# Performance work log

Measured on AMD Instinct MI355X. Metric: run time of the kernel, lower is better.

The kernel has to match this reference:

```python
import jax, jax.numpy as jnp
import numpy as np

LN_EPS = 1e-5


def setup_inputs() -> dict:
    key = jax.random.key(0)
    ks = jax.random.split(key, 5)
    B, L, D, H = 4, 4096, 2048, 16
    s = 0.02  # keep activations in a sane range for fp32
    return {
        "x": jax.random.normal(ks[0], (B, L, D), jnp.float32),
        "Wq": jax.random.normal(ks[1], (D, D), jnp.float32) * s,
        "Wv": jax.random.normal(ks[2], (D, D), jnp.float32) * s,
        "Wg": jax.random.normal(ks[3], (D, D), jnp.float32) * s,
        "Wo": jax.random.normal(ks[4], (D, D), jnp.float32) * s,
        "beta": jnp.full((H,), -0.2, jnp.float32),  # module init: _beta = -0.2
        "ln_w": jnp.ones((D,), jnp.float32),
        "ln_b": jnp.zeros((D,), jnp.float32),
    }


def _retention_scan(v, lam):
    # v: (B, L, H, Dh); lam: (H,). state_t = lam * state_{t-1} + v_t
    B, L, H, Dh = v.shape
    a = jnp.broadcast_to(lam[None, None, :, None], (B, L, H, 1))

    def combine(c1, c2):
        a1, b1 = c1
        a2, b2 = c2
        return (a1 * a2, b1 * a2 + b2)

    _, state = jax.lax.associative_scan(combine, (a, v), axis=1)
    return state  # (B, L, H, Dh)


def reference(x, Wq, Wv, Wg, Wo, beta, ln_w, ln_b):
    B, L, D = x.shape
    H = beta.shape[0]
    Dh = D // H
    # bias-free projections (torch Linear: x @ W.T)
    q = (x @ Wq.T).reshape(B, L, H, Dh)
    v = (x @ Wv.T).reshape(B, L, H, Dh)
    lam = jax.nn.sigmoid(beta)  # per-head decay, (H,)
    state = _retention_scan(v, lam)  # decay-weighted cumulative sum
    y = (q * state).reshape(B, L, D)
    # LayerNorm over d_model
    mu = jnp.mean(y, axis=-1, keepdims=True)
    var = jnp.mean(jnp.square(y - mu), axis=-1, keepdims=True)
    y = (y - mu) * jax.lax.rsqrt(var + LN_EPS) * ln_w + ln_b
    # SiLU gate
    y = y * jax.nn.silu(x @ Wg.T)
    return y @ Wo.T
```

## Files before the change

### kernel.cpp

```cpp
#include <hip/hip_runtime.h>

#define BATCH 4
#define SEQ   4096
#define DMODEL 2048
#define NHEAD 16
#define DHEAD 128
#define MROWS (BATCH*SEQ)
#define LC    128
#define NCH   (SEQ/LC)

typedef unsigned short ushort_t;
typedef __bf16 v8bf __attribute__((ext_vector_type(8)));
typedef float  f32x4 __attribute__((ext_vector_type(4)));

__device__ __forceinline__ float b2f(ushort_t h) {
    return __uint_as_float(((unsigned)h) << 16);
}
__device__ __forceinline__ ushort_t f2b(float f) {
    unsigned u = __float_as_uint(f);
    return (ushort_t)((u + 0x7fffu + ((u >> 16) & 1u)) >> 16);
}

__global__ void cast_f32_bf16(const float* __restrict__ in, ushort_t* __restrict__ out, int n) {
    int i = (blockIdx.x * blockDim.x + threadIdx.x) * 8;
    const int stride = gridDim.x * blockDim.x * 8;
    for (; i < n; i += stride) {
        float4 a = *(const float4*)(in + i);
        float4 b = *(const float4*)(in + i + 4);
        ushort_t o[8] = {f2b(a.x), f2b(a.y), f2b(a.z), f2b(a.w),
                         f2b(b.x), f2b(b.y), f2b(b.z), f2b(b.w)};
        *(uint4*)(out + i) = *(const uint4*)o;
    }
}

__global__ void cast_weights(const float* __restrict__ w0, const float* __restrict__ w1,
                             const float* __restrict__ w2, const float* __restrict__ w3,
                             ushort_t* __restrict__ o0, ushort_t* __restrict__ o1,
                             ushort_t* __restrict__ o2, ushort_t* __restrict__ o3) {
    const int wsel = blockIdx.y;
    const float* src = wsel == 0 ? w0 : wsel == 1 ? w1 : wsel == 2 ? w2 : w3;
    ushort_t* dst    = wsel == 0 ? o0 : wsel == 1 ? o1 : wsel == 2 ? o2 : o3;
    const int n = DMODEL * DMODEL;
    int i = (blockIdx.x * blockDim.x + threadIdx.x) * 8;
    const int stride = gridDim.x * blockDim.x * 8;
    for (; i < n; i += stride) {
        float4 a = *(const float4*)(src + i);
        float4 b = *(const float4*)(src + i + 4);
        ushort_t o[8] = {f2b(a.x), f2b(a.y), f2b(a.z), f2b(a.w),
                         f2b(b.x), f2b(b.y), f2b(b.z), f2b(b.w)};
        *(uint4*)(dst + i) = *(const uint4*)o;
    }
}


#define GLL(src, dstoff) __builtin_amdgcn_global_load_lds( \
    (const __attribute__((address_space(1))) void*)(src), \
    (__attribute__((address_space(3))) void*)((char*)lds + (dstoff)), 16, 0, 0)

#define STG_A(buf, half, kt) do { \
    GLL(pA + ((half) * 128 +  0) * (size_t)K + (kt), (buf) * 65536 + (half) * 16384 + wid * 1024); \
    GLL(pA + ((half) * 128 + 64) * (size_t)K + (kt), (buf) * 65536 + (half) * 16384 + wid * 1024 + 8192); } while (0)
#define STG_B(buf, half, kt) do { \
    GLL(pB + ((half) * 128 +  0) * (size_t)K + (kt), (buf) * 65536 + 32768 + (half) * 16384 + wid * 1024); \
    GLL(pB + ((half) * 128 + 64) * (size_t)K + (kt), (buf) * 65536 + 32768 + (half) * 16384 + wid * 1024 + 8192); } while (0)

#define DSRD4(dst, off) do { \
    const ushort_t* _p = lds + (off); \
    dst[0] = *(const v8bf*)_p;          dst[1] = *(const v8bf*)(_p + 1024); \
    dst[2] = *(const v8bf*)(_p + 2048); dst[3] = *(const v8bf*)(_p + 3072); } while (0)

#define VMW(n) asm volatile("s_waitcnt vmcnt(" #n ")" ::: "memory")
#define BAR()  __builtin_amdgcn_s_barrier()

#define MM(mh, va, vb) do { \
    __builtin_amdgcn_s_setprio(1); \
    _Pragma("unroll") \
    for (int _m = 0; _m < 4; ++_m) \
        _Pragma("unroll") \
        for (int _n = 0; _n < 4; ++_n) \
            acc[(mh) * 4 + _m][_n] = __builtin_amdgcn_mfma_f32_16x16x32_bf16( \
                va[_m], vb[_n], acc[(mh) * 4 + _m][_n], 0, 0, 0); \
    __builtin_amdgcn_s_setprio(0); \
} while (0)

template<int N, int EPI>
__global__ __launch_bounds__(512, 2) void gemm8(const ushort_t* __restrict__ A,
                                                const ushort_t* __restrict__ Bm,
                                                ushort_t* __restrict__ o0,
                                                ushort_t* __restrict__ o1,
                                                ushort_t* __restrict__ o2,
                                                float* __restrict__ of) {
    constexpr int K  = DMODEL;
    constexpr int NT = K / 64;
    constexpr int NBN = N / 256;
    constexpr int NWG = (MROWS / 256) * NBN;
    extern __shared__ ushort_t lds[];

    int wg = blockIdx.x;
    wg = (wg & 7) * (NWG / 8) + (wg >> 3);
    const int tm = (wg / NBN) * 256;
    const int tn = (wg % NBN) * 256;

    const int tid  = threadIdx.x;
    const int lane = tid & 63;
    const int wid  = tid >> 6;
    const int wr   = wid >> 2;
    const int wc   = wid & 3;

    const int rs = wid * 8 + (lane >> 3);
    const int cs = ((lane & 7) ^ ((lane >> 3) & 7)) * 8;
    const ushort_t* pA = A  + (size_t)(tm + rs) * K + cs;
    const ushort_t* pB = Bm + (size_t)(tn + rs) * K + cs;

    const int q  = lane >> 4;
    const int l4 = lane & 15;
    const int sx = l4 & 7;
    const int abase0 = (wr * 128 + l4) * 64 + ((q ^ sx)) * 8;
    const int abase1 = (wr * 128 + l4) * 64 + (((4 + q) ^ sx)) * 8;
    const int bbase0 = 16384 + (wc * 64 + l4) * 64 + ((q ^ sx)) * 8;
    const int bbase1 = 16384 + (wc * 64 + l4) * 64 + (((4 + q) ^ sx)) * 8;

    f32x4 acc[8][4] = {};
    v8bf a00[4], a10[4], a01[4], a11[4], b0[4], b1[4];

    STG_A(0, 0, 0); STG_A(0, 1, 0); STG_B(0, 0, 0); STG_B(0, 1, 0);

    for (int t = 0; t < NT - 1; ++t) {
        const int cur = t & 1, nxt = cur ^ 1;
        const int ktn = (t + 1) * 64;
        const int cb = cur * 32768;
        STG_A(nxt, 0, ktn);
        VMW(2);
        BAR();
        DSRD4(a00, cb + abase0);
        DSRD4(b0,  cb + bbase0);
        DSRD4(a10, cb + abase0 + 4096);
        MM(0, a00, b0);
        STG_A(nxt, 1, ktn);
        DSRD4(a01, cb + abase1);
        DSRD4(b1,  cb + bbase1);
        MM(1, a10, b0);
        STG_B(nxt, 0, ktn);
        DSRD4(a11, cb + abase1 + 4096);
        MM(0, a01, b1);
        STG_B(nxt, 1, ktn);
        MM(1, a11, b1);
        BAR();
    }
    {
        const int cb = ((NT - 1) & 1) * 32768;
        VMW(0);
        BAR();
        DSRD4(a00, cb + abase0);
        DSRD4(b0,  cb + bbase0);
        DSRD4(a10, cb + abase0 + 4096);
        MM(0, a00, b0);
        DSRD4(a01, cb + abase1);
        DSRD4(b1,  cb + bbase1);
        MM(1, a10, b0);
        DSRD4(a11, cb + abase1 + 4096);
        MM(0, a01, b1);
        MM(1, a11, b1);
    }

    const int cr = (lane >> 4) * 4;
    const int cc = lane & 15;
    if constexpr (EPI == 0) {
        ushort_t* out = (tn < 2048) ? o0 : (tn < 4096 ? o1 : o2);
        const int nc0 = tn & 2047;
#pragma unroll
        for (int m = 0; m < 8; ++m) {
            const int r0 = tm + wr * 128 + m * 16 + cr;
#pragma unroll
            for (int n = 0; n < 4; ++n) {
                const int c = nc0 + wc * 64 + n * 16 + cc;
#pragma unroll
                for (int j = 0; j < 4; ++j)
                    out[(size_t)(r0 + j) * 2048 + c] = f2b(acc[m][n][j]);
            }
        }
    } else {
#pragma unroll
        for (int m = 0; m < 8; ++m) {
            const int r0 = tm + wr * 128 + m * 16 + cr;
#pragma unroll
            for (int n = 0; n < 4; ++n) {
                const int c = tn + wc * 64 + n * 16 + cc;
#pragma unroll
                for (int j = 0; j < 4; ++j)
                    of[(size_t)(r0 + j) * N + c] = acc[m][n][j];
            }
        }
    }
}

__global__ void scan_pass1(const ushort_t* __restrict__ v, const float* __restrict__ beta,
                           float* __restrict__ cf) {
    const int chunk = blockIdx.x, h = blockIdx.y, b = blockIdx.z;
    const int dh = threadIdx.x;
    const float lam = 1.f / (1.f + __expf(-beta[h]));
    size_t idx = ((size_t)(b * SEQ + chunk * LC) * NHEAD + h) * DHEAD + dh;
    float s = 0.f;
#pragma unroll 4
    for (int l = 0; l < LC; ++l) {
        s = fmaf(s, lam, b2f(v[idx]));
        idx += DMODEL;
    }
    cf[(((size_t)(b * NHEAD + h) * NCH) + chunk) * DHEAD + dh] = s;
}

__global__ void scan_pass2(float* __restrict__ cf, const float* __restrict__ beta) {
    const int t = blockIdx.x * blockDim.x + threadIdx.x;
    const int dh = t & 127;
    const int bh = t >> 7;
    const int h = bh & 15;
    const float lam = 1.f / (1.f + __expf(-beta[h]));
    float lamLc = lam;
#pragma unroll
    for (int i = 0; i < 7; ++i) lamLc *= lamLc;
    float carry = 0.f;
    for (int c = 0; c < NCH; ++c) {
        const size_t i = ((size_t)bh * NCH + c) * DHEAD + dh;
        const float val = cf[i];
        cf[i] = carry;
        carry = fmaf(carry, lamLc, val);
    }
}

__global__ void scan_pass3(const ushort_t* __restrict__ v, const ushort_t* __restrict__ q,
                           const float* __restrict__ beta, const float* __restrict__ cf,
                           ushort_t* __restrict__ y) {
    const int chunk = blockIdx.x, h = blockIdx.y, b = blockIdx.z;
    const int dh = threadIdx.x;
    const float lam = 1.f / (1.f + __expf(-beta[h]));
    float s = cf[(((size_t)(b * NHEAD + h) * NCH) + chunk) * DHEAD + dh];
    size_t idx = ((size_t)(b * SEQ + chunk * LC) * NHEAD + h) * DHEAD + dh;
#pragma unroll 4
    for (int l = 0; l < LC; ++l) {
        s = fmaf(s, lam, b2f(v[idx]));
        y[idx] = f2b(b2f(q[idx]) * s);
        idx += DMODEL;
    }
}

__global__ __launch_bounds__(256) void ln_gate(const ushort_t* __restrict__ y,
                                               const ushort_t* g,
                                               const float* __restrict__ lnw,
                                               const float* __restrict__ lnb,
                                               ushort_t* t) {
    const int row = blockIdx.x;
    const int tid = threadIdx.x;
    const size_t base = (size_t)row * DMODEL + tid * 8;

    float yv[8];
    {
        const uint4 raw = *(const uint4*)(y + base);
        const ushort_t* p = (const ushort_t*)&raw;
#pragma unroll
        for (int j = 0; j < 8; ++j) yv[j] = b2f(p[j]);
    }
    float s = 0.f, ss = 0.f;
#pragma unroll
    for (int j = 0; j < 8; ++j) { s += yv[j]; ss += yv[j] * yv[j]; }

#pragma unroll
    for (int o = 32; o > 0; o >>= 1) { s += __shfl_down(s, o); ss += __shfl_down(ss, o); }
    __shared__ float red[8];
    const int wid = tid >> 6, lane = tid & 63;
    if (lane == 0) { red[wid] = s; red[4 + wid] = ss; }
    __syncthreads();
    s  = red[0] + red[1] + red[2] + red[3];
    ss = red[4] + red[5] + red[6] + red[7];

    const float mu = s * (1.f / DMODEL);
    const float var = ss * (1.f / DMODEL) - mu * mu;
    const float rs = rsqrtf(var + 1e-5f);

    const int c0 = tid * 8;
    float4 w0 = *(const float4*)(lnw + c0), w1 = *(const float4*)(lnw + c0 + 4);
    float4 b0 = *(const float4*)(lnb + c0), b1 = *(const float4*)(lnb + c0 + 4);
    const float wv[8] = {w0.x, w0.y, w0.z, w0.w, w1.x, w1.y, w1.z, w1.w};
    const float bv[8] = {b0.x, b0.y, b0.z, b0.w, b1.x, b1.y, b1.z, b1.w};

    float gv[8];
    {
        const uint4 raw = *(const uint4*)(g + base);
        const ushort_t* p = (const ushort_t*)&raw;
#pragma unroll
        for (int j = 0; j < 8; ++j) gv[j] = b2f(p[j]);
    }

    ushort_t out[8];
#pragma unroll
    for (int j = 0; j < 8; ++j) {
        const float tv = (yv[j] - mu) * rs * wv[j] + bv[j];
        const float sil = gv[j] / (1.f + __expf(-gv[j]));
        out[j] = f2b(tv * sil);
    }
    *(uint4*)(t + base) = *(const uint4*)out;
}

#define OFF_XB  ((size_t)0)
#define OFF_WC  (OFF_XB + (size_t)MROWS*DMODEL*2)
#define OFF_WOB (OFF_WC + (size_t)3*DMODEL*DMODEL*2)
#define OFF_G   (OFF_WOB + (size_t)DMODEL*DMODEL*2)
#define OFF_CF  (OFF_G + (size_t)MROWS*DMODEL*2)
#define OFF_END (OFF_CF + (size_t)BATCH*NHEAD*NCH*DHEAD*4)

extern "C" void kernel_launch(void* const* d_in, const int* in_sizes, int n_in,
                              void* d_out, int out_size, void* d_ws, size_t ws_size,
                              hipStream_t stream) {
    if (ws_size < OFF_END) return;

    const float* x    = (const float*)d_in[0];
    const float* Wq   = (const float*)d_in[1];
    const float* Wv   = (const float*)d_in[2];
    const float* Wg   = (const float*)d_in[3];
    const float* Wo   = (const float*)d_in[4];
    const float* beta = (const float*)d_in[5];
    const float* lnw  = (const float*)d_in[6];
    const float* lnb  = (const float*)d_in[7];

    char* ws = (char*)d_ws;
    ushort_t* xb  = (ushort_t*)(ws + OFF_XB);
    ushort_t* Wc  = (ushort_t*)(ws + OFF_WC);
    ushort_t* Wob = (ushort_t*)(ws + OFF_WOB);
    ushort_t* g   = (ushort_t*)(ws + OFF_G);
    float*    cf  = (float*)(ws + OFF_CF);

    ushort_t* q = (ushort_t*)d_out;
    ushort_t* v = q + (size_t)MROWS * DMODEL;
    ushort_t* y = xb;
    ushort_t* t = g;

    const int DD = DMODEL * DMODEL;

    (void)hipFuncSetAttribute((const void*)gemm8<3 * DMODEL, 0>,
                              hipFuncAttributeMaxDynamicSharedMemorySize, 131072);
    (void)hipFuncSetAttribute((const void*)gemm8<DMODEL, 1>,
                              hipFuncAttributeMaxDynamicSharedMemorySize, 131072);

    cast_f32_bf16<<<2048, 256, 0, stream>>>(x, xb, MROWS * DMODEL);
    cast_weights<<<dim3(256, 4), 256, 0, stream>>>(Wq, Wv, Wg, Wo,
                                                   Wc, Wc + DD, Wc + 2 * DD, Wob);

    gemm8<3 * DMODEL, 0><<<(MROWS / 256) * (3 * DMODEL / 256), 512, 131072, stream>>>(
        xb, Wc, q, v, g, nullptr);

    scan_pass1<<<dim3(NCH, NHEAD, BATCH), DHEAD, 0, stream>>>(v, beta, cf);
    scan_pass2<<<(BATCH * NHEAD * DHEAD) / 256, 256, 0, stream>>>(cf, beta);
    scan_pass3<<<dim3(NCH, NHEAD, BATCH), DHEAD, 0, stream>>>(v, q, beta, cf, y);

    ln_gate<<<MROWS, 256, 0, stream>>>(y, g, lnw, lnb, t);

    gemm8<DMODEL, 1><<<(MROWS / 256) * (DMODEL / 256), 512, 131072, stream>>>(
        t, Wob, nullptr, nullptr, nullptr, (float*)d_out);
}
```

Baseline: 628.0 us.

## Switch GEMM to 32x32x16 MFMA and fuse scan pass3 with LayerNorm gate

The GEMM inner loop now uses 32x32x16 bf16 MFMA tiles with a new LDS read pattern and epilogue mapping, which issues fewer MFMA instructions and fewer LDS reads per K step. The third scan pass and the LayerNorm/SiLU-gate kernel are merged into one kernel that keeps full rows in a 512-thread block. This removes the y intermediate round-trip through HBM and one launch. The scan chunk length is halved to restore parallelism for that fused kernel, with a per-row block reduction and two barriers per timestep as the cost. The chunk carry buffer is moved into the now-unused x-bf16 workspace region.

Measured after the change: 728.1 us. +15.9%, slower.

```diff
diff --git a/kernel.cpp b/kernel.cpp
--- a/kernel.cpp
+++ b/kernel.cpp
@@ -6,12 +6,12 @@
 #define NHEAD 16
 #define DHEAD 128
 #define MROWS (BATCH*SEQ)
-#define LC    128
+#define LC    64
 #define NCH   (SEQ/LC)
 
 typedef unsigned short ushort_t;
-typedef __bf16 v8bf __attribute__((ext_vector_type(8)));
-typedef float  f32x4 __attribute__((ext_vector_type(4)));
+typedef __bf16 v8bf  __attribute__((ext_vector_type(8)));
+typedef float  f32x16 __attribute__((ext_vector_type(16)));
 
 __device__ __forceinline__ float b2f(ushort_t h) {
     return __uint_as_float(((unsigned)h) << 16);
@@ -64,22 +64,26 @@
     GLL(pB + ((half) * 128 +  0) * (size_t)K + (kt), (buf) * 65536 + 32768 + (half) * 16384 + wid * 1024); \
     GLL(pB + ((half) * 128 + 64) * (size_t)K + (kt), (buf) * 65536 + 32768 + (half) * 16384 + wid * 1024 + 8192); } while (0)
 
-#define DSRD4(dst, off) do { \
-    const ushort_t* _p = lds + (off); \
-    dst[0] = *(const v8bf*)_p;          dst[1] = *(const v8bf*)(_p + 1024); \
-    dst[2] = *(const v8bf*)(_p + 2048); dst[3] = *(const v8bf*)(_p + 3072); } while (0)
+#define RD6(FA, FB, ks) do { \
+    const int _sl = ((((ks) * 2 + khalf) ^ sx7)) * 8; \
+    const ushort_t* _pa = lds + cb + aw + _sl; \
+    FA[0] = *(const v8bf*)_pa;          FA[1] = *(const v8bf*)(_pa + 2048); \
+    FA[2] = *(const v8bf*)(_pa + 4096); FA[3] = *(const v8bf*)(_pa + 6144); \
+    const ushort_t* _pb = lds + cb + bw + _sl; \
+    FB[0] = *(const v8bf*)_pb;          FB[1] = *(const v8bf*)(_pb + 2048); \
+} while (0)
 
 #define VMW(n) asm volatile("s_waitcnt vmcnt(" #n ")" ::: "memory")
 #define BAR()  __builtin_amdgcn_s_barrier()
 
-#define MM(mh, va, vb) do { \
+#define MM8(FA, FB) do { \
     __builtin_amdgcn_s_setprio(1); \
     _Pragma("unroll") \
     for (int _m = 0; _m < 4; ++_m) \
         _Pragma("unroll") \
-        for (int _n = 0; _n < 4; ++_n) \
-            acc[(mh) * 4 + _m][_n] = __builtin_amdgcn_mfma_f32_16x16x32_bf16( \
-                va[_m], vb[_n], acc[(mh) * 4 + _m][_n], 0, 0, 0); \
+        for (int _n = 0; _n < 2; ++_n) \
+            acc[_m][_n] = __builtin_amdgcn_mfma_f32_32x32x16_bf16( \
+                FA[_m], FB[_n], acc[_m][_n], 0, 0, 0); \
     __builtin_amdgcn_s_setprio(0); \
 } while (0)
 
@@ -112,16 +116,15 @@
     const ushort_t* pA = A  + (size_t)(tm + rs) * K + cs;
     const ushort_t* pB = Bm + (size_t)(tn + rs) * K + cs;
 
-    const int q  = lane >> 4;
-    const int l4 = lane & 15;
-    const int sx = l4 & 7;
-    const int abase0 = (wr * 128 + l4) * 64 + ((q ^ sx)) * 8;
-    const int abase1 = (wr * 128 + l4) * 64 + (((4 + q) ^ sx)) * 8;
-    const int bbase0 = 16384 + (wc * 64 + l4) * 64 + ((q ^ sx)) * 8;
-    const int bbase1 = 16384 + (wc * 64 + l4) * 64 + (((4 + q) ^ sx)) * 8;
-
-    f32x4 acc[8][4] = {};
-    v8bf a00[4], a10[4], a01[4], a11[4], b0[4], b1[4];
+    const int r31   = lane & 31;
+    const int khalf = lane >> 5;
+    const int sx7   = r31 & 7;
+    const int aw = (wr * 128 + r31) * 64;
+    const int bw = 16384 + (wc * 64 + r31) * 64;
+
+    f32x16 acc[4][2] = {};
+    v8bf Ae[4], Ao[4];
+    v8bf Be[2], Bo[2];
 
     STG_A(0, 0, 0); STG_A(0, 1, 0); STG_B(0, 0, 0); STG_B(0, 1, 0);
 
@@ -132,63 +135,61 @@
         STG_A(nxt, 0, ktn);
         VMW(2);
         BAR();
-        DSRD4(a00, cb + abase0);
-        DSRD4(b0,  cb + bbase0);
-        DSRD4(a10, cb + abase0 + 4096);
-        MM(0, a00, b0);
+        RD6(Ae, Be, 0);
+        RD6(Ao, Bo, 1);
+        MM8(Ae, Be);
         STG_A(nxt, 1, ktn);
-        DSRD4(a01, cb + abase1);
-        DSRD4(b1,  cb + bbase1);
-        MM(1, a10, b0);
+        RD6(Ae, Be, 2);
+        MM8(Ao, Bo);
         STG_B(nxt, 0, ktn);
-        DSRD4(a11, cb + abase1 + 4096);
-        MM(0, a01, b1);
+        RD6(Ao, Bo, 3);
+        MM8(Ae, Be);
         STG_B(nxt, 1, ktn);
-        MM(1, a11, b1);
+        MM8(Ao, Bo);
         BAR();
     }
     {
         const int cb = ((NT - 1) & 1) * 32768;
         VMW(0);
         BAR();
-        DSRD4(a00, cb + abase0);
-        DSRD4(b0,  cb + bbase0);
-        DSRD4(a10, cb + abase0 + 4096);
-        MM(0, a00, b0);
-        DSRD4(a01, cb + abase1);
-        DSRD4(b1,  cb + bbase1);
-        MM(1, a10, b0);
-        DSRD4(a11, cb + abase1 + 4096);
-        MM(0, a01, b1);
-        MM(1, a11, b1);
-    }
-
-    const int cr = (lane >> 4) * 4;
-    const int cc = lane & 15;
+        RD6(Ae, Be, 0);
+        RD6(Ao, Bo, 1);
+        MM8(Ae, Be);
+        RD6(Ae, Be, 2);
+        MM8(Ao, Bo);
+        RD6(Ao, Bo, 3);
+        MM8(Ae, Be);
+        MM8(Ao, Bo);
+    }
+
     if constexpr (EPI == 0) {
         ushort_t* out = (tn < 2048) ? o0 : (tn < 4096 ? o1 : o2);
         const int nc0 = tn & 2047;
 #pragma unroll
-        for (int m = 0; m < 8; ++m) {
-            const int r0 = tm + wr * 128 + m * 16 + cr;
-#pragma unroll
-            for (int n = 0; n < 4; ++n) {
-                const int c = nc0 + wc * 64 + n * 16 + cc;
-#pragma unroll
-                for (int j = 0; j < 4; ++j)
-                    out[(size_t)(r0 + j) * 2048 + c] = f2b(acc[m][n][j]);
+        for (int m = 0; m < 4; ++m) {
+            const int r0 = tm + wr * 128 + m * 32 + khalf * 4;
+#pragma unroll
+            for (int n = 0; n < 2; ++n) {
+                const int c = nc0 + wc * 64 + n * 32 + r31;
+#pragma unroll
+                for (int reg = 0; reg < 16; ++reg) {
+                    const int row = r0 + (reg & 3) + 8 * (reg >> 2);
+                    out[(size_t)row * 2048 + c] = f2b(acc[m][n][reg]);
+                }
             }
         }
     } else {
 #pragma unroll
-        for (int m = 0; m < 8; ++m) {
-            const int r0 = tm + wr * 128 + m * 16 + cr;
-#pragma unroll
-            for (int n = 0; n < 4; ++n) {
-                const int c = tn + wc * 64 + n * 16 + cc;
-#pragma unroll
-                for (int j = 0; j < 4; ++j)
-                    of[(size_t)(r0 + j) * N + c] = acc[m][n][j];
+        for (int m = 0; m < 4; ++m) {
+            const int r0 = tm + wr * 128 + m * 32 + khalf * 4;
+#pragma unroll
+            for (int n = 0; n < 2; ++n) {
+                const int c = tn + wc * 64 + n * 32 + r31;
+#pragma unroll
+                for (int reg = 0; reg < 16; ++reg) {
+                    const int row = r0 + (reg & 3) + 8 * (reg >> 2);
+                    of[(size_t)row * N + c] = acc[m][n][reg];
+                }
             }
         }
     }
@@ -217,7 +218,7 @@
     const float lam = 1.f / (1.f + __expf(-beta[h]));
     float lamLc = lam;
 #pragma unroll
-    for (int i = 0; i < 7; ++i) lamLc *= lamLc;
+    for (int i = 0; i < 6; ++i) lamLc *= lamLc;
     float carry = 0.f;
     for (int c = 0; c < NCH; ++c) {
         const size_t i = ((size_t)bh * NCH + c) * DHEAD + dh;
@@ -227,85 +228,85 @@
     }
 }
 
-__global__ void scan_pass3(const ushort_t* __restrict__ v, const ushort_t* __restrict__ q,
-                           const float* __restrict__ beta, const float* __restrict__ cf,
-                           ushort_t* __restrict__ y) {
-    const int chunk = blockIdx.x, h = blockIdx.y, b = blockIdx.z;
-    const int dh = threadIdx.x;
+__global__ __launch_bounds__(512) void scan3_ln_gate(const ushort_t* __restrict__ v,
+                                                     const ushort_t* __restrict__ q,
+                                                     const ushort_t* g,
+                                                     const float* __restrict__ beta,
+                                                     const float* __restrict__ cf,
+                                                     const float* __restrict__ lnw,
+                                                     const float* __restrict__ lnb,
+                                                     ushort_t* t) {
+    const int chunk = blockIdx.x;
+    const int b     = blockIdx.y;
+    const int tid   = threadIdx.x;
+    const int h     = tid >> 5;
+    const int col   = (h << 7) + ((tid & 31) << 2);
     const float lam = 1.f / (1.f + __expf(-beta[h]));
-    float s = cf[(((size_t)(b * NHEAD + h) * NCH) + chunk) * DHEAD + dh];
-    size_t idx = ((size_t)(b * SEQ + chunk * LC) * NHEAD + h) * DHEAD + dh;
-#pragma unroll 4
+
+    float s0, s1, s2, s3;
+    {
+        const float* c0 = cf + ((size_t)(b * NHEAD + h) * NCH + chunk) * DHEAD + ((tid & 31) << 2);
+        s0 = c0[0]; s1 = c0[1]; s2 = c0[2]; s3 = c0[3];
+    }
+    const float w0 = lnw[col], w1 = lnw[col + 1], w2 = lnw[col + 2], w3 = lnw[col + 3];
+    const float e0 = lnb[col], e1 = lnb[col + 1], e2 = lnb[col + 2], e3 = lnb[col + 3];
+
+    __shared__ float red[16];
+    size_t idx = (size_t)(b * SEQ + chunk * LC) * DMODEL + col;
+
     for (int l = 0; l < LC; ++l) {
-        s = fmaf(s, lam, b2f(v[idx]));
-        y[idx] = f2b(b2f(q[idx]) * s);
+        const uint2 vv = *(const uint2*)(v + idx);
+        s0 = fmaf(s0, lam, b2f((ushort_t)(vv.x & 0xffff)));
+        s1 = fmaf(s1, lam, b2f((ushort_t)(vv.x >> 16)));
+        s2 = fmaf(s2, lam, b2f((ushort_t)(vv.y & 0xffff)));
+        s3 = fmaf(s3, lam, b2f((ushort_t)(vv.y >> 16)));
+        const uint2 qv = *(const uint2*)(q + idx);
+        const float y0 = b2f((ushort_t)(qv.x & 0xffff)) * s0;
+        const float y1 = b2f((ushort_t)(qv.x >> 16)) * s1;
+        const float y2 = b2f((ushort_t)(qv.y & 0xffff)) * s2;
+        const float y3 = b2f((ushort_t)(qv.y >> 16)) * s3;
+
+        float ps  = y0 + y1 + y2 + y3;
+        float pss = y0 * y0 + y1 * y1 + y2 * y2 + y3 * y3;
+#pragma unroll
+        for (int o = 32; o > 0; o >>= 1) {
+            ps  += __shfl_down(ps, o);
+            pss += __shfl_down(pss, o);
+        }
+        const int wv = tid >> 6;
+        if ((tid & 63) == 0) { red[wv] = ps; red[8 + wv] = pss; }
+        __syncthreads();
+        float S = 0.f, SS = 0.f;
+#pragma unroll
+        for (int k = 0; k < 8; ++k) { S += red[k]; SS += red[8 + k]; }
+
+        const float mu  = S * (1.f / DMODEL);
+        const float var = SS * (1.f / DMODEL) - mu * mu;
+        const float rsr = rsqrtf(var + 1e-5f);
+
+        const uint2 gv = *(const uint2*)(g + idx);
+        const float g0 = b2f((ushort_t)(gv.x & 0xffff));
+        const float g1 = b2f((ushort_t)(gv.x >> 16));
+        const float g2 = b2f((ushort_t)(gv.y & 0xffff));
+        const float g3 = b2f((ushort_t)(gv.y >> 16));
+
+        ushort_t o[4];
+        o[0] = f2b(((y0 - mu) * rsr * w0 + e0) * (g0 / (1.f + __expf(-g0))));
+        o[1] = f2b(((y1 - mu) * rsr * w1 + e1) * (g1 / (1.f + __expf(-g1))));
+        o[2] = f2b(((y2 - mu) * rsr * w2 + e2) * (g2 / (1.f + __expf(-g2))));
+        o[3] = f2b(((y3 - mu) * rsr * w3 + e3) * (g3 / (1.f + __expf(-g3))));
+        *(uint2*)(t + idx) = *(const uint2*)o;
+
+        __syncthreads();
         idx += DMODEL;
     }
-}
-
-__global__ __launch_bounds__(256) void ln_gate(const ushort_t* __restrict__ y,
-                                               const ushort_t* g,
-                                               const float* __restrict__ lnw,
-                                               const float* __restrict__ lnb,
-                                               ushort_t* t) {
-    const int row = blockIdx.x;
-    const int tid = threadIdx.x;
-    const size_t base = (size_t)row * DMODEL + tid * 8;
-
-    float yv[8];
-    {
-        const uint4 raw = *(const uint4*)(y + base);
-        const ushort_t* p = (const ushort_t*)&raw;
-#pragma unroll
-        for (int j = 0; j < 8; ++j) yv[j] = b2f(p[j]);
-    }
-    float s = 0.f, ss = 0.f;
-#pragma unroll
-    for (int j = 0; j < 8; ++j) { s += yv[j]; ss += yv[j] * yv[j]; }
-
-#pragma unroll
-    for (int o = 32; o > 0; o >>= 1) { s += __shfl_down(s, o); ss += __shfl_down(ss, o); }
-    __shared__ float red[8];
-    const int wid = tid >> 6, lane = tid & 63;
-    if (lane == 0) { red[wid] = s; red[4 + wid] = ss; }
-    __syncthreads();
-    s  = red[0] + red[1] + red[2] + red[3];
-    ss = red[4] + red[5] + red[6] + red[7];
-
-    const float mu = s * (1.f / DMODEL);
-    const float var = ss * (1.f / DMODEL) - mu * mu;
-    const float rs = rsqrtf(var + 1e-5f);
-
-    const int c0 = tid * 8;
-    float4 w0 = *(const float4*)(lnw + c0), w1 = *(const float4*)(lnw + c0 + 4);
-    float4 b0 = *(const float4*)(lnb + c0), b1 = *(const float4*)(lnb + c0 + 4);
-    const float wv[8] = {w0.x, w0.y, w0.z, w0.w, w1.x, w1.y, w1.z, w1.w};
-    const float bv[8] = {b0.x, b0.y, b0.z, b0.w, b1.x, b1.y, b1.z, b1.w};
-
-    float gv[8];
-    {
-        const uint4 raw = *(const uint4*)(g + base);
-        const ushort_t* p = (const ushort_t*)&raw;
-#pragma unroll
-        for (int j = 0; j < 8; ++j) gv[j] = b2f(p[j]);
-    }
-
-    ushort_t out[8];
-#pragma unroll
-    for (int j = 0; j < 8; ++j) {
-        const float tv = (yv[j] - mu) * rs * wv[j] + bv[j];
-        const float sil = gv[j] / (1.f + __expf(-gv[j]));
-        out[j] = f2b(tv * sil);
-    }
-    *(uint4*)(t + base) = *(const uint4*)out;
 }
 
 #define OFF_XB  ((size_t)0)
 #define OFF_WC  (OFF_XB + (size_t)MROWS*DMODEL*2)
 #define OFF_WOB (OFF_WC + (size_t)3*DMODEL*DMODEL*2)
 #define OFF_G   (OFF_WOB + (size_t)DMODEL*DMODEL*2)
-#define OFF_CF  (OFF_G + (size_t)MROWS*DMODEL*2)
-#define OFF_END (OFF_CF + (size_t)BATCH*NHEAD*NCH*DHEAD*4)
+#define OFF_END (OFF_G + (size_t)MROWS*DMODEL*2)
 
 extern "C" void kernel_launch(void* const* d_in, const int* in_sizes, int n_in,
                               void* d_out, int out_size, void* d_ws, size_t ws_size,
@@ -326,11 +327,10 @@
     ushort_t* Wc  = (ushort_t*)(ws + OFF_WC);
     ushort_t* Wob = (ushort_t*)(ws + OFF_WOB);
     ushort_t* g   = (ushort_t*)(ws + OFF_G);
-    float*    cf  = (float*)(ws + OFF_CF);
+    float*    cf  = (float*)(ws + OFF_XB);
 
     ushort_t* q = (ushort_t*)d_out;
     ushort_t* v = q + (size_t)MROWS * DMODEL;
-    ushort_t* y = xb;
     ushort_t* t = g;
 
     const int DD = DMODEL * DMODEL;
@@ -349,9 +349,7 @@
 
     scan_pass1<<<dim3(NCH, NHEAD, BATCH), DHEAD, 0, stream>>>(v, beta, cf);
     scan_pass2<<<(BATCH * NHEAD * DHEAD) / 256, 256, 0, stream>>>(cf, beta);
-    scan_pass3<<<dim3(NCH, NHEAD, BATCH), DHEAD, 0, stream>>>(v, q, beta, cf, y);
-
-    ln_gate<<<MROWS, 256, 0, stream>>>(y, g, lnw, lnb, t);
+    scan3_ln_gate<<<dim3(NCH, BATCH), 512, 0, stream>>>(v, q, g, beta, cf, lnw, lnb, t);
 
     gemm8<DMODEL, 1><<<(MROWS / 256) * (DMODEL / 256), 512, 131072, stream>>>(
         t, Wob, nullptr, nullptr, nullptr, (float*)d_out);
```
